# Performance work log

Measured on AMD Instinct MI355X. Metric: run time of the kernel, lower is better.

The kernel has to match this reference:

```python
import jax, jax.numpy as jnp
import numpy as np

N, C = 131072, 128
NUM_PREDICTORS = 8


def setup_inputs() -> dict:
    key = jax.random.key(0)
    ks = jax.random.split(key, 9)
    d = {f"outputs{i+1}": jax.random.normal(ks[i], (N, C), dtype=jnp.float32) for i in range(7)}
    d["mimic"] = jax.random.normal(ks[7], (N, C), dtype=jnp.float32)
    d["targets"] = jax.random.randint(ks[8], (N,), 0, C, dtype=jnp.int32)
    d["n_test"] = N
    return d


def _margin(x, targets):
    # x: [N, C]; top-2 margin if the target logit is the max, else 0 (ties by value equality, as in torch code)
    top2, _ = jax.lax.top_k(x, 2)                                  # [N, 2]
    tval = jnp.take_along_axis(x, targets[:, None], axis=1)[:, 0]  # [N]
    return jnp.where(tval == top2[:, 0], top2[:, 0] - top2[:, 1], jnp.zeros((), x.dtype))


def reference(outputs1, outputs2, outputs3, outputs4, outputs5, outputs6, outputs7, mimic, targets, n_test):
    T = 2.0
    preds = [outputs1, outputs2, outputs3, outputs4, outputs5, outputs6, outputs7, mimic]
    # [N, 8] margins, one column per predictor
    margins = jnp.stack([_margin(p, targets) for p in preds], axis=1)
    out_threshold = jax.nn.softmax(margins / T, axis=1)            # softmax over the 8 predictors per sample
    max_preds = jnp.max(jnp.stack(preds[:7], axis=0))              # global max over outputs1..7
    return max_preds, out_threshold
```

## Files before the change

kernel.cpp:

```cpp
#include <hip/hip_runtime.h>
#include <cfloat>

constexpr int kN = 131072;
constexpr int kC = 128;
constexpr int kIters = 8;
constexpr int kRowsPerIter = 8;
constexpr int kRowsPerBlock = kIters * kRowsPerIter;

__device__ __forceinline__ unsigned fmap(float f) {
    unsigned b = __float_as_uint(f);
    return (b & 0x80000000u) ? ~b : (b | 0x80000000u);
}

__device__ __forceinline__ void top2_merge(float& m1, float& m2, float o1, float o2) {
    const float lo = fminf(m1, o1);
    m1 = fmaxf(m1, o1);
    m2 = fmaxf(fmaxf(m2, o2), lo);
}

__global__ __launch_bounds__(256, 8) void margins_kernel(
    const float* __restrict__ p0, const float* __restrict__ p1,
    const float* __restrict__ p2, const float* __restrict__ p3,
    const float* __restrict__ p4, const float* __restrict__ p5,
    const float* __restrict__ p6, const float* __restrict__ p7,
    const int* __restrict__ targets, float* __restrict__ out,
    unsigned* __restrict__ gmax_ws)
{
    __shared__ unsigned blockmax;
    const int t = threadIdx.x;
    if (t == 0) blockmax = 0u;
    __syncthreads();

    const float* preds[8] = {p0, p1, p2, p3, p4, p5, p6, p7};

    const int c    = t & 31;
    const int rown = t >> 5;
    float gm = -FLT_MAX;

    for (int it = 0; it < kIters; ++it) {
        const int row = blockIdx.x * kRowsPerBlock + it * kRowsPerIter + rown;
        const int tgt = targets[row];
        const size_t off = (size_t)row * kC + c * 4;

        const int ts   = tgt & 3;
        const int srcl = (t & 32) + (tgt >> 2);

        float marg[8];

#pragma unroll
        for (int h = 0; h < 2; ++h) {
            float4 v[4];
#pragma unroll
            for (int j = 0; j < 4; ++j) v[j] = *(const float4*)(preds[h * 4 + j] + off);
            __builtin_amdgcn_sched_barrier(0);

#pragma unroll
            for (int j = 0; j < 4; ++j) {
                const float4 w = v[j];
                float a1 = fmaxf(w.x, w.y), a2 = fminf(w.x, w.y);
                float b1 = fmaxf(w.z, w.w), b2 = fminf(w.z, w.w);
                float m1 = fmaxf(a1, b1);
                float m2 = fmaxf(fminf(a1, b1), fmaxf(a2, b2));
                float tv = (ts == 0) ? w.x : (ts == 1) ? w.y : (ts == 2) ? w.z : w.w;
#pragma unroll
                for (int mask = 1; mask <= 16; mask <<= 1) {
                    const float o1 = __shfl_xor(m1, mask);
                    const float o2 = __shfl_xor(m2, mask);
                    top2_merge(m1, m2, o1, o2);
                }
                tv = __shfl(tv, srcl);
                marg[h * 4 + j] = (tv == m1) ? (m1 - m2) : 0.0f;
                if (h * 4 + j < 7) gm = fmaxf(gm, m1);
            }
        }

        const float mm = fmaxf(
            fmaxf(fmaxf(marg[0], marg[1]), fmaxf(marg[2], marg[3])),
            fmaxf(fmaxf(marg[4], marg[5]), fmaxf(marg[6], marg[7])));
        const float e0 = __expf((marg[0] - mm) * 0.5f);
        const float e1 = __expf((marg[1] - mm) * 0.5f);
        const float e2 = __expf((marg[2] - mm) * 0.5f);
        const float e3 = __expf((marg[3] - mm) * 0.5f);
        const float e4 = __expf((marg[4] - mm) * 0.5f);
        const float e5 = __expf((marg[5] - mm) * 0.5f);
        const float e6 = __expf((marg[6] - mm) * 0.5f);
        const float e7 = __expf((marg[7] - mm) * 0.5f);
        const float s  = e0 + e1 + e2 + e3 + e4 + e5 + e6 + e7;
        const float num = (c == 0) ? e0 : (c == 1) ? e1 : (c == 2) ? e2 :
                          (c == 3) ? e3 : (c == 4) ? e4 : (c == 5) ? e5 :
                          (c == 6) ? e6 : e7;
        if (c < 8) out[1 + (size_t)row * 8 + c] = num / s;
    }

    gm = fmaxf(gm, __shfl_xor(gm, 32));
    if ((t & 63) == 0) atomicMax(&blockmax, fmap(gm));
    __syncthreads();
    if (t == 0) atomicMax(gmax_ws, blockmax);
}

__global__ void finalize_kernel(const unsigned* __restrict__ gmax_ws,
                                float* __restrict__ out)
{
    unsigned u = *gmax_ws;
    unsigned b = (u & 0x80000000u) ? (u & 0x7FFFFFFFu) : ~u;
    out[0] = __uint_as_float(b);
}

extern "C" void kernel_launch(void* const* d_in, const int* in_sizes, int n_in,
                              void* d_out, int out_size, void* d_ws, size_t ws_size,
                              hipStream_t stream) {
    const float* p0 = (const float*)d_in[0];
    const float* p1 = (const float*)d_in[1];
    const float* p2 = (const float*)d_in[2];
    const float* p3 = (const float*)d_in[3];
    const float* p4 = (const float*)d_in[4];
    const float* p5 = (const float*)d_in[5];
    const float* p6 = (const float*)d_in[6];
    const float* p7 = (const float*)d_in[7];
    const int* targets = (const int*)d_in[8];
    float* out = (float*)d_out;
    unsigned* ws = (unsigned*)d_ws;

    hipMemsetAsync(ws, 0, sizeof(unsigned), stream);

    dim3 grid(kN / kRowsPerBlock), block(256);
    margins_kernel<<<grid, block, 0, stream>>>(p0, p1, p2, p3, p4, p5, p6, p7,
                                               targets, out, ws);
    finalize_kernel<<<1, 1, 0, stream>>>(ws, out);
}
```

Before: 474.7 us.

## Remap rows to 16-lane groups, double-buffer loads, use DPP reductions

Reassigns work so that each 16-lane group handles one row, with each lane loading two float4s. Loads are software-pipelined across 32 steps (predictor × row iteration) with double-buffered registers. Cross-lane top-2 and target-value reductions use DPP row moves instead of ds_bpermute shuffles. Margins are staged through LDS so the softmax is computed by all lanes with a multiply by the reciprocal. In exchange it adds LDS traffic, raises register pressure from the unrolled pipeline, and relies on a wave-local LDS write-then-read without an explicit barrier.

```diff
diff --git a/kernel.cpp b/kernel.cpp
--- a/kernel.cpp
+++ b/kernel.cpp
@@ -3,13 +3,17 @@
 
 constexpr int kN = 131072;
 constexpr int kC = 128;
-constexpr int kIters = 8;
-constexpr int kRowsPerIter = 8;
-constexpr int kRowsPerBlock = kIters * kRowsPerIter;
+constexpr int kRowsPerBlock = 64;
 
 __device__ __forceinline__ unsigned fmap(float f) {
     unsigned b = __float_as_uint(f);
     return (b & 0x80000000u) ? ~b : (b | 0x80000000u);
+}
+
+template<int CTRL>
+__device__ __forceinline__ float dppmov(float x) {
+    return __int_as_float(__builtin_amdgcn_update_dpp(
+        __float_as_int(x), __float_as_int(x), CTRL, 0xF, 0xF, false));
 }
 
 __device__ __forceinline__ void top2_merge(float& m1, float& m2, float o1, float o2) {
@@ -26,74 +30,110 @@
     const int* __restrict__ targets, float* __restrict__ out,
     unsigned* __restrict__ gmax_ws)
 {
+    __shared__ float marg_lds[kRowsPerBlock][9];
     __shared__ unsigned blockmax;
+
     const int t = threadIdx.x;
     if (t == 0) blockmax = 0u;
     __syncthreads();
 
     const float* preds[8] = {p0, p1, p2, p3, p4, p5, p6, p7};
 
-    const int c    = t & 31;
-    const int rown = t >> 5;
+    const int l   = t & 63;
+    const int w   = t >> 6;
+    const int myl = l & 15;
+    const int rg  = l >> 4;
+    const int R0  = blockIdx.x * kRowsPerBlock + w * 16;
+
+    const size_t base_off = ((size_t)(R0 + rg) * kC + myl * 4) * sizeof(float);
+
+    int tg[4];
+#pragma unroll
+    for (int it = 0; it < 4; ++it) tg[it] = targets[R0 + it * 4 + rg];
+
     float gm = -FLT_MAX;
 
-    for (int it = 0; it < kIters; ++it) {
-        const int row = blockIdx.x * kRowsPerBlock + it * kRowsPerIter + rown;
-        const int tgt = targets[row];
-        const size_t off = (size_t)row * kC + c * 4;
-
-        const int ts   = tgt & 3;
-        const int srcl = (t & 32) + (tgt >> 2);
-
-        float marg[8];
+    float4 A[2], B[2];
+    {
+        const char* p = (const char*)preds[0] + base_off;
+        A[0] = *(const float4*)p;
+        B[0] = *(const float4*)(p + 256);
+    }
 
 #pragma unroll
-        for (int h = 0; h < 2; ++h) {
-            float4 v[4];
-#pragma unroll
-            for (int j = 0; j < 4; ++j) v[j] = *(const float4*)(preds[h * 4 + j] + off);
-            __builtin_amdgcn_sched_barrier(0);
+    for (int g = 0; g < 32; ++g) {
+        const int j  = g >> 2;
+        const int it = g & 3;
 
-#pragma unroll
-            for (int j = 0; j < 4; ++j) {
-                const float4 w = v[j];
-                float a1 = fmaxf(w.x, w.y), a2 = fminf(w.x, w.y);
-                float b1 = fmaxf(w.z, w.w), b2 = fminf(w.z, w.w);
-                float m1 = fmaxf(a1, b1);
-                float m2 = fmaxf(fminf(a1, b1), fmaxf(a2, b2));
-                float tv = (ts == 0) ? w.x : (ts == 1) ? w.y : (ts == 2) ? w.z : w.w;
-#pragma unroll
-                for (int mask = 1; mask <= 16; mask <<= 1) {
-                    const float o1 = __shfl_xor(m1, mask);
-                    const float o2 = __shfl_xor(m2, mask);
-                    top2_merge(m1, m2, o1, o2);
-                }
-                tv = __shfl(tv, srcl);
-                marg[h * 4 + j] = (tv == m1) ? (m1 - m2) : 0.0f;
-                if (h * 4 + j < 7) gm = fmaxf(gm, m1);
-            }
+        if (g < 31) {
+            const int jn  = (g + 1) >> 2;
+            const int itn = (g + 1) & 3;
+            const char* p = (const char*)preds[jn] + base_off
+                          + (size_t)itn * 4 * kC * sizeof(float);
+            A[(g + 1) & 1] = *(const float4*)p;
+            B[(g + 1) & 1] = *(const float4*)(p + 256);
         }
+        __builtin_amdgcn_sched_barrier(0);
 
-        const float mm = fmaxf(
-            fmaxf(fmaxf(marg[0], marg[1]), fmaxf(marg[2], marg[3])),
-            fmaxf(fmaxf(marg[4], marg[5]), fmaxf(marg[6], marg[7])));
-        const float e0 = __expf((marg[0] - mm) * 0.5f);
-        const float e1 = __expf((marg[1] - mm) * 0.5f);
-        const float e2 = __expf((marg[2] - mm) * 0.5f);
-        const float e3 = __expf((marg[3] - mm) * 0.5f);
-        const float e4 = __expf((marg[4] - mm) * 0.5f);
-        const float e5 = __expf((marg[5] - mm) * 0.5f);
-        const float e6 = __expf((marg[6] - mm) * 0.5f);
-        const float e7 = __expf((marg[7] - mm) * 0.5f);
-        const float s  = e0 + e1 + e2 + e3 + e4 + e5 + e6 + e7;
-        const float num = (c == 0) ? e0 : (c == 1) ? e1 : (c == 2) ? e2 :
-                          (c == 3) ? e3 : (c == 4) ? e4 : (c == 5) ? e5 :
-                          (c == 6) ? e6 : e7;
-        if (c < 8) out[1 + (size_t)row * 8 + c] = num / s;
+        const float4 va = A[g & 1];
+        const float4 vb = B[g & 1];
+
+        const int  tt = tg[it];
+        const bool mt = (((tt >> 2) & 15) == myl);
+        const float4 hv = (tt & 64) ? vb : va;
+        const int el = tt & 3;
+        float tvc = (el == 0) ? hv.x : (el == 1) ? hv.y : (el == 2) ? hv.z : hv.w;
+        tvc = mt ? tvc : -FLT_MAX;
+
+        float a1 = fmaxf(va.x, va.y), a2 = fminf(va.x, va.y);
+        float b1 = fmaxf(va.z, va.w), b2 = fminf(va.z, va.w);
+        const float mA1 = fmaxf(a1, b1);
+        const float mA2 = fmaxf(fminf(a1, b1), fmaxf(a2, b2));
+        a1 = fmaxf(vb.x, vb.y); a2 = fminf(vb.x, vb.y);
+        b1 = fmaxf(vb.z, vb.w); b2 = fminf(vb.z, vb.w);
+        const float mB1 = fmaxf(a1, b1);
+        const float mB2 = fmaxf(fminf(a1, b1), fmaxf(a2, b2));
+        float m1 = mA1, m2 = mA2;
+        top2_merge(m1, m2, mB1, mB2);
+
+        { const float o1 = dppmov<0xB1>(m1),  o2 = dppmov<0xB1>(m2);  top2_merge(m1, m2, o1, o2); }
+        { const float o1 = dppmov<0x4E>(m1),  o2 = dppmov<0x4E>(m2);  top2_merge(m1, m2, o1, o2); }
+        { const float o1 = dppmov<0x124>(m1), o2 = dppmov<0x124>(m2); top2_merge(m1, m2, o1, o2); }
+        { const float o1 = dppmov<0x128>(m1), o2 = dppmov<0x128>(m2); top2_merge(m1, m2, o1, o2); }
+
+        tvc = fmaxf(tvc, dppmov<0xB1>(tvc));
+        tvc = fmaxf(tvc, dppmov<0x4E>(tvc));
+        tvc = fmaxf(tvc, dppmov<0x124>(tvc));
+        tvc = fmaxf(tvc, dppmov<0x128>(tvc));
+
+        const float margin = (tvc == m1) ? (m1 - m2) : 0.0f;
+        if (myl == 0) marg_lds[w * 16 + it * 4 + rg][j] = margin;
+        if (j < 7) gm = fmaxf(gm, m1);
     }
 
+    {
+        const int rr = l >> 2;
+        const int q  = l & 3;
+        float m[8];
+#pragma unroll
+        for (int jj = 0; jj < 8; ++jj) m[jj] = marg_lds[w * 16 + rr][jj];
+        float mm = m[0];
+#pragma unroll
+        for (int jj = 1; jj < 8; ++jj) mm = fmaxf(mm, m[jj]);
+        float e[8], s = 0.0f;
+#pragma unroll
+        for (int jj = 0; jj < 8; ++jj) { e[jj] = __expf((m[jj] - mm) * 0.5f); s += e[jj]; }
+        const float inv = 1.0f / s;
+        const float o0 = ((q == 0) ? e[0] : (q == 1) ? e[2] : (q == 2) ? e[4] : e[6]) * inv;
+        const float o1 = ((q == 0) ? e[1] : (q == 1) ? e[3] : (q == 2) ? e[5] : e[7]) * inv;
+        const size_t ob = 1 + ((size_t)(blockIdx.x * kRowsPerBlock + w * 16 + rr)) * 8 + q * 2;
+        out[ob]     = o0;
+        out[ob + 1] = o1;
+    }
+
+    gm = fmaxf(gm, __shfl_xor(gm, 16));
     gm = fmaxf(gm, __shfl_xor(gm, 32));
-    if ((t & 63) == 0) atomicMax(&blockmax, fmap(gm));
+    if (l == 0) atomicMax(&blockmax, fmap(gm));
     __syncthreads();
     if (t == 0) atomicMax(gmax_ws, blockmax);
 }
```

Result: faster. 440.9 us (-7.1%).
